# Optimization experiments

Measured on AMD Instinct MI355X. Metric: run time of the kernel, lower is better.

Reference implementation:

```python
import jax, jax.numpy as jnp
import numpy as np

LN_EPS = 1e-5  # torch.nn.LayerNorm default


def setup_inputs() -> dict:
    key = jax.random.key(0)
    ks = jax.random.split(key, 6)
    b, e, c, h, w, m = 4, 16, 256, 32, 64, 1024
    return {
        "x": jax.random.normal(ks[0], (b, e, c, h, w), dtype=jnp.float32),
        "ln_w": jnp.ones((c, h, w), dtype=jnp.float32),
        "ln_b": jnp.zeros((c, h, w), dtype=jnp.float32),
        "w_in": jax.random.normal(ks[1], (c, m), dtype=jnp.float32) * (1.0 / np.sqrt(c)),
        "b_in": jax.random.normal(ks[2], (m,), dtype=jnp.float32) * 0.01,
        "w_out": jax.random.normal(ks[3], (m, c), dtype=jnp.float32) * (1.0 / np.sqrt(m)),
        "b_out": jax.random.normal(ks[4], (c,), dtype=jnp.float32) * 0.01,
        "gamma": jnp.full((c,), 1e-6, dtype=jnp.float32),
    }


def reference(x, ln_w, ln_b, w_in, b_in, w_out, b_out, gamma):
    # LayerNorm over the last 3 dims (c, h, w) with affine params of shape (c, h, w)
    mu = jnp.mean(x, axis=(-3, -2, -1), keepdims=True)
    var = jnp.var(x, axis=(-3, -2, -1), keepdims=True)  # biased, matches torch
    y = (x - mu) * jax.lax.rsqrt(var + LN_EPS)
    y = y * ln_w + ln_b  # broadcast (c,h,w) over (b,e,...)

    # b e c h w -> b e h w c
    y = jnp.moveaxis(y, 2, -1)
    t = jax.nn.gelu(y @ w_in + b_in, approximate=False)  # torch GELU is exact erf
    t = (t @ w_out + b_out) * gamma  # layer scale on channel dim

    # b e h w c -> b e c h w, residual add
    return x + jnp.moveaxis(t, -1, 2)
```

## Files before the change

### kernel.cpp

```cpp
#include <hip/hip_runtime.h>
#include <math.h>

#define NS 64
#define CD 256
#define HW 2048
#define MD 1024
#define SAMPLE (CD * HW)
#define LN_EPS 1e-5f

#define PB 64
#define MC 32
#define NCH (MD / MC)

typedef float f32x4 __attribute__((ext_vector_type(4)));
typedef long i64;
typedef long i64x2 __attribute__((ext_vector_type(2)));

__device__ __forceinline__ int swz(int p) {
  int k = (p ^ (p >> 2)) & 15;
  return ((k & 7) << 4) | (k & 8);
}

__device__ __forceinline__ void gl_lds16(const unsigned char* g, unsigned char* l) {
  __builtin_amdgcn_global_load_lds(
      (const __attribute__((address_space(1))) unsigned char*)g,
      (__attribute__((address_space(3))) unsigned char*)l, 16, 0, 0);
}

__global__ __launch_bounds__(256) void k_prep_stats(
    const float* __restrict__ x, const float* __restrict__ w_in,
    const float* __restrict__ w_out, unsigned char* __restrict__ w_in8p,
    unsigned char* __restrict__ w_out8p, double* __restrict__ partial) {
  if (blockIdx.x < 512) {
    int s = blockIdx.x >> 3, sl = blockIdx.x & 7;
    const float4* p = (const float4*)(x + (size_t)s * SAMPLE + (size_t)sl * 65536);
    double sum = 0.0, ssq = 0.0;
    for (int i = 0; i < 64; ++i) {
      float4 v = p[i * 256 + threadIdx.x];
      sum += (double)v.x + (double)v.y + (double)v.z + (double)v.w;
      ssq += (double)v.x * v.x + (double)v.y * v.y + (double)v.z * v.z + (double)v.w * v.w;
    }
    for (int off = 32; off; off >>= 1) {
      sum += __shfl_down(sum, off);
      ssq += __shfl_down(ssq, off);
    }
    __shared__ double red[4][2];
    int wv = threadIdx.x >> 6, ln = threadIdx.x & 63;
    if (ln == 0) { red[wv][0] = sum; red[wv][1] = ssq; }
    __syncthreads();
    if (threadIdx.x == 0) {
      for (int i = 1; i < 4; ++i) { sum += red[i][0]; ssq += red[i][1]; }
      partial[blockIdx.x * 2] = sum;
      partial[blockIdx.x * 2 + 1] = ssq;
    }
  } else {
    int id = (blockIdx.x - 512) * 256 + threadIdx.x;
    int off = id << 2;
    int ch = off >> 13, r = off & 8191;
    int h = r >> 12; r &= 4095;
    int pr = r >> 10; r &= 1023;
    int lane = r >> 4; r &= 15;
    int lo = r >> 3, j0 = r & 7;
    int kk = pr * 2 + lo;
    if (id < 65536) {
      int m = ch * 32 + h * 16 + (lane & 15);
      int c0 = kk * 32 + (lane >> 4) * 8 + j0;
      float a = w_in[(size_t)(c0 + 0) * MD + m];
      float b = w_in[(size_t)(c0 + 1) * MD + m];
      float c = w_in[(size_t)(c0 + 2) * MD + m];
      float d = w_in[(size_t)(c0 + 3) * MD + m];
      int rr = __builtin_amdgcn_cvt_pk_fp8_f32(a, b, 0, false);
      rr = __builtin_amdgcn_cvt_pk_fp8_f32(c, d, rr, true);
      *(int*)(w_in8p + off) = rr;
    } else {
      off = (id - 65536) << 2;
      ch = off >> 13; r = off & 8191;
      h = r >> 12; r &= 4095;
      pr = r >> 10; r &= 1023;
      lane = r >> 4; r &= 15;
      lo = r >> 3; j0 = r & 7;
      int ct = pr * 2 + lo;
      int c = h * 128 + ct * 16 + (lane & 15);
      int m0 = ch * 32 + (lane >> 4) * 8 + j0;
      float a = w_out[(size_t)(m0 + 0) * CD + c];
      float b = w_out[(size_t)(m0 + 1) * CD + c];
      float cc = w_out[(size_t)(m0 + 2) * CD + c];
      float d = w_out[(size_t)(m0 + 3) * CD + c];
      int rr = __builtin_amdgcn_cvt_pk_fp8_f32(a, b, 0, false);
      rr = __builtin_amdgcn_cvt_pk_fp8_f32(cc, d, rr, true);
      *(int*)(w_out8p + off) = rr;
    }
  }
}

__global__ __launch_bounds__(512, 6) void k_fused(
    const float* __restrict__ x, const float* __restrict__ ln_w, const float* __restrict__ ln_b,
    const float* __restrict__ b_in, const float* __restrict__ b_out, const float* __restrict__ gamma,
    const unsigned char* __restrict__ w_in8p, const unsigned char* __restrict__ w_out8p,
    const double* __restrict__ partial, float* __restrict__ out) {
  __shared__ unsigned char smem[45056];
  unsigned char* Ysh = smem + 8192;

  const int tid = threadIdx.x;
  const int lane = tid & 63, l15 = lane & 15, l4 = lane >> 4;
  const int wv = tid >> 6;
  const int q = wv >> 1, h = wv & 1;
  const int s = blockIdx.x >> 5;
  const int p0 = (blockIdx.x & 31) * PB;
  const size_t xbase = (size_t)s * SAMPLE;

  double sum = 0.0, ssq = 0.0;
  #pragma unroll
  for (int i = 0; i < 8; ++i) {
    sum += partial[s * 16 + i * 2];
    ssq += partial[s * 16 + i * 2 + 1];
  }
  double mean = sum / (double)SAMPLE;
  double var = ssq / (double)SAMPLE - mean * mean;
  const float rstd = (float)(1.0 / sqrt(var + (double)LN_EPS));
  const float a_ln = rstd, c_ln = -(float)mean * rstd;

  gl_lds16(w_in8p + wv * 1024 + lane * 16, smem + 24576 + wv * 1024);
  gl_lds16(w_out8p + wv * 1024 + lane * 16, smem + wv * 1024);

  #pragma unroll
  for (int it = 0; it < 2; ++it) {
    int bid = it * 512 + tid;
    int c0 = (bid >> 4) * 4, pp = (bid & 15) * 4;
    float yv[4][4];
    #pragma unroll
    for (int i = 0; i < 4; ++i) {
      size_t off = (size_t)(c0 + i) * HW + p0 + pp;
      float4 xv = *(const float4*)(x + xbase + off);
      float4 lw = *(const float4*)(ln_w + off);
      float4 lb = *(const float4*)(ln_b + off);
      yv[i][0] = fmaf(fmaf(xv.x, a_ln, c_ln), lw.x, lb.x);
      yv[i][1] = fmaf(fmaf(xv.y, a_ln, c_ln), lw.y, lb.y);
      yv[i][2] = fmaf(fmaf(xv.z, a_ln, c_ln), lw.z, lb.z);
      yv[i][3] = fmaf(fmaf(xv.w, a_ln, c_ln), lw.w, lb.w);
    }
    #pragma unroll
    for (int j = 0; j < 4; ++j) {
      int p = pp + j;
      int r = __builtin_amdgcn_cvt_pk_fp8_f32(yv[0][j], yv[1][j], 0, false);
      r = __builtin_amdgcn_cvt_pk_fp8_f32(yv[2][j], yv[3][j], r, true);
      *(int*)&Ysh[p * 256 + (c0 ^ swz(p))] = r;
    }
  }

  const int strip = q * 16;
  const int pY = strip + l15;
  const int sY = swz(pY);
  f32x4 acc2[8] = {};

  __syncthreads();

  i64 breg[8];
  #pragma unroll
  for (int kk = 0; kk < 8; ++kk)
    breg[kk] = *(const i64*)&Ysh[pY * 256 + ((kk * 32 + l4 * 8) ^ sY)];

  __syncthreads();

  const int exw = ((((h * 16 + l4 * 4) >> 3) ^ (l15 >> 2)) << 3) + ((l4 & 1) * 4);
  const int exw_off = 40960 + q * 512 + l15 * 32 + exw;
  const int exr_off = 40960 + q * 512 + l15 * 32 + ((l4 ^ (l15 >> 2)) << 3);

  for (int ch = 0; ch < NCH; ++ch) {
    if (ch) __syncthreads();

    if (ch + 1 < NCH) {
      const size_t co = (size_t)(ch + 1) * 8192;
      gl_lds16(w_in8p + co + wv * 1024 + lane * 16,
               smem + 24576 + ((ch + 1) & 1) * 8192 + wv * 1024);
      gl_lds16(w_out8p + co + wv * 1024 + lane * 16,
               smem + ((ch + 1) % 3) * 8192 + wv * 1024);
    }

    i64 a2 = 0;
    if (ch) a2 = *(const i64*)(smem + ((ch - 1) & 1) * 2048 + exr_off);

    const unsigned char* W1 = smem + 24576 + (ch & 1) * 8192 + h * 4096;
    f32x4 acc1a = {}, acc1b = {};
    __builtin_amdgcn_s_setprio(1);
    #pragma unroll
    for (int kp = 0; kp < 4; ++kp) {
      i64x2 w = *(const i64x2*)&W1[kp * 1024 + lane * 16];
      acc1a = __builtin_amdgcn_mfma_f32_16x16x32_fp8_fp8(w.x, breg[kp * 2], acc1a, 0, 0, 0);
      acc1b = __builtin_amdgcn_mfma_f32_16x16x32_fp8_fp8(w.y, breg[kp * 2 + 1], acc1b, 0, 0, 0);
    }
    __builtin_amdgcn_s_setprio(0);

    {
      const float4 bi = *(const float4*)&b_in[ch * 32 + h * 16 + l4 * 4];
      float g[4];
      #pragma unroll
      for (int r = 0; r < 4; ++r) {
        float t = acc1a[r] + acc1b[r] + ((const float*)&bi)[r];
        g[r] = t * __builtin_amdgcn_rcpf(1.0f + __expf(-1.702f * t));
      }
      int pk = __builtin_amdgcn_cvt_pk_fp8_f32(g[0], g[1], 0, false);
      pk = __builtin_amdgcn_cvt_pk_fp8_f32(g[2], g[3], pk, true);
      *(int*)(smem + (ch & 1) * 2048 + exw_off) = pk;
    }

    if (ch) {
      const unsigned char* W2 = smem + ((ch - 1) % 3) * 8192 + h * 4096;
      __builtin_amdgcn_s_setprio(1);
      #pragma unroll
      for (int cp = 0; cp < 4; ++cp) {
        i64x2 w = *(const i64x2*)&W2[cp * 1024 + lane * 16];
        acc2[cp * 2] = __builtin_amdgcn_mfma_f32_16x16x32_fp8_fp8(a2, w.x, acc2[cp * 2], 0, 0, 0);
        acc2[cp * 2 + 1] = __builtin_amdgcn_mfma_f32_16x16x32_fp8_fp8(a2, w.y, acc2[cp * 2 + 1], 0, 0, 0);
      }
      __builtin_amdgcn_s_setprio(0);
    }
  }

  __syncthreads();
  {
    const i64 a2 = *(const i64*)(smem + ((NCH - 1) & 1) * 2048 + exr_off);
    const unsigned char* W2 = smem + ((NCH - 1) % 3) * 8192 + h * 4096;
    #pragma unroll
    for (int cp = 0; cp < 4; ++cp) {
      i64x2 w = *(const i64x2*)&W2[cp * 1024 + lane * 16];
      acc2[cp * 2] = __builtin_amdgcn_mfma_f32_16x16x32_fp8_fp8(a2, w.x, acc2[cp * 2], 0, 0, 0);
      acc2[cp * 2 + 1] = __builtin_amdgcn_mfma_f32_16x16x32_fp8_fp8(a2, w.y, acc2[cp * 2 + 1], 0, 0, 0);
    }
  }

  #pragma unroll
  for (int cti = 0; cti < 8; ++cti) {
    int cc = h * 128 + cti * 16 + l15;
    float gm = gamma[cc], bo = b_out[cc];
    int p = p0 + strip + l4 * 4;
    size_t off = xbase + (size_t)cc * HW + p;
    float4 xv = *(const float4*)(x + off);
    float4 o;
    #pragma unroll
    for (int r = 0; r < 4; ++r)
      ((float*)&o)[r] = ((const float*)&xv)[r] + gm * (acc2[cti][r] + bo);
    *(float4*)(out + off) = o;
  }
}

extern "C" void kernel_launch(void* const* d_in, const int* in_sizes, int n_in,
                              void* d_out, int out_size, void* d_ws, size_t ws_size,
                              hipStream_t stream) {
  const float* x = (const float*)d_in[0];
  const float* ln_w = (const float*)d_in[1];
  const float* ln_b = (const float*)d_in[2];
  const float* w_in = (const float*)d_in[3];
  const float* b_in = (const float*)d_in[4];
  const float* w_out = (const float*)d_in[5];
  const float* b_out = (const float*)d_in[6];
  const float* gamma = (const float*)d_in[7];
  float* out = (float*)d_out;

  char* ws = (char*)d_ws;
  unsigned char* w_in8p = (unsigned char*)ws;
  unsigned char* w_out8p = (unsigned char*)(ws + 262144);
  double* partial = (double*)(ws + 524288);

  k_prep_stats<<<1024, 256, 0, stream>>>(x, w_in, w_out, w_in8p, w_out8p, partial);

  k_fused<<<2048, 512, 0, stream>>>(x, ln_w, ln_b, b_in, b_out, gamma,
                                    w_in8p, w_out8p, partial, out);
}
```

Before: 169.8 us.

## Load w_out fragments from global directly and keep Y tile resident in LDS

Stops staging the packed fp8 w_out chunks through a triple-buffered LDS region and has each lane load its w_out fragments straight from global memory (L2-cached) each chunk. Half of the Y operand registers are now re-read from LDS inside the loop instead of being held, so Ysh must stay live and the post-load barrier is dropped. The Y tile moves to offset 0, which shrinks LDS from 45056 to 36864 bytes to raise occupancy and reduce register pressure. In exchange the loop issues global loads with higher latency on the GEMM2 path and adds LDS reads in GEMM1.

```diff
diff --git a/kernel.cpp b/kernel.cpp
--- a/kernel.cpp
+++ b/kernel.cpp
@@ -55,14 +55,14 @@
     }
   } else {
     int id = (blockIdx.x - 512) * 256 + threadIdx.x;
-    int off = id << 2;
-    int ch = off >> 13, r = off & 8191;
-    int h = r >> 12; r &= 4095;
-    int pr = r >> 10; r &= 1023;
-    int lane = r >> 4; r &= 15;
-    int lo = r >> 3, j0 = r & 7;
-    int kk = pr * 2 + lo;
     if (id < 65536) {
+      int off = id << 2;
+      int ch = off >> 13, r = off & 8191;
+      int h = r >> 12; r &= 4095;
+      int pr = r >> 10; r &= 1023;
+      int lane = r >> 4; r &= 15;
+      int lo = r >> 3, j0 = r & 7;
+      int kk = pr * 2 + lo;
       int m = ch * 32 + h * 16 + (lane & 15);
       int c0 = kk * 32 + (lane >> 4) * 8 + j0;
       float a = w_in[(size_t)(c0 + 0) * MD + m];
@@ -73,12 +73,12 @@
       rr = __builtin_amdgcn_cvt_pk_fp8_f32(c, d, rr, true);
       *(int*)(w_in8p + off) = rr;
     } else {
-      off = (id - 65536) << 2;
-      ch = off >> 13; r = off & 8191;
-      h = r >> 12; r &= 4095;
-      pr = r >> 10; r &= 1023;
-      lane = r >> 4; r &= 15;
-      lo = r >> 3; j0 = r & 7;
+      int off = (id - 65536) << 2;
+      int ch = off >> 13, r = off & 8191;
+      int h = r >> 12; r &= 4095;
+      int pr = r >> 10; r &= 1023;
+      int lane = r >> 4; r &= 15;
+      int lo = r >> 3, j0 = r & 7;
       int ct = pr * 2 + lo;
       int c = h * 128 + ct * 16 + (lane & 15);
       int m0 = ch * 32 + (lane >> 4) * 8 + j0;
@@ -98,8 +98,8 @@
     const float* __restrict__ b_in, const float* __restrict__ b_out, const float* __restrict__ gamma,
     const unsigned char* __restrict__ w_in8p, const unsigned char* __restrict__ w_out8p,
     const double* __restrict__ partial, float* __restrict__ out) {
-  __shared__ unsigned char smem[45056];
-  unsigned char* Ysh = smem + 8192;
+  __shared__ unsigned char smem[36864];
+  unsigned char* Ysh = smem;
 
   const int tid = threadIdx.x;
   const int lane = tid & 63, l15 = lane & 15, l4 = lane >> 4;
@@ -120,8 +120,7 @@
   const float rstd = (float)(1.0 / sqrt(var + (double)LN_EPS));
   const float a_ln = rstd, c_ln = -(float)mean * rstd;
 
-  gl_lds16(w_in8p + wv * 1024 + lane * 16, smem + 24576 + wv * 1024);
-  gl_lds16(w_out8p + wv * 1024 + lane * 16, smem + wv * 1024);
+  gl_lds16(w_in8p + wv * 1024 + lane * 16, smem + 16384 + wv * 1024);
 
   #pragma unroll
   for (int it = 0; it < 2; ++it) {
@@ -155,39 +154,50 @@
 
   __syncthreads();
 
-  i64 breg[8];
-  #pragma unroll
-  for (int kk = 0; kk < 8; ++kk)
+  i64 breg[4];
+  #pragma unroll
+  for (int kk = 0; kk < 4; ++kk)
     breg[kk] = *(const i64*)&Ysh[pY * 256 + ((kk * 32 + l4 * 8) ^ sY)];
 
-  __syncthreads();
-
   const int exw = ((((h * 16 + l4 * 4) >> 3) ^ (l15 >> 2)) << 3) + ((l4 & 1) * 4);
-  const int exw_off = 40960 + q * 512 + l15 * 32 + exw;
-  const int exr_off = 40960 + q * 512 + l15 * 32 + ((l4 ^ (l15 >> 2)) << 3);
+  const int exw_off = 32768 + q * 512 + l15 * 32 + exw;
+  const int exr_off = 32768 + q * 512 + l15 * 32 + ((l4 ^ (l15 >> 2)) << 3);
+
+  const unsigned char* W2g = w_out8p + h * 4096 + lane * 16;
 
   for (int ch = 0; ch < NCH; ++ch) {
     if (ch) __syncthreads();
 
     if (ch + 1 < NCH) {
-      const size_t co = (size_t)(ch + 1) * 8192;
-      gl_lds16(w_in8p + co + wv * 1024 + lane * 16,
-               smem + 24576 + ((ch + 1) & 1) * 8192 + wv * 1024);
-      gl_lds16(w_out8p + co + wv * 1024 + lane * 16,
-               smem + ((ch + 1) % 3) * 8192 + wv * 1024);
-    }
-
+      gl_lds16(w_in8p + (size_t)(ch + 1) * 8192 + wv * 1024 + lane * 16,
+               smem + 16384 + ((ch + 1) & 1) * 8192 + wv * 1024);
+    }
+
+    i64x2 w2p[4];
     i64 a2 = 0;
-    if (ch) a2 = *(const i64*)(smem + ((ch - 1) & 1) * 2048 + exr_off);
-
-    const unsigned char* W1 = smem + 24576 + (ch & 1) * 8192 + h * 4096;
+    if (ch) {
+      #pragma unroll
+      for (int cp = 0; cp < 4; ++cp)
+        w2p[cp] = *(const i64x2*)(W2g + (size_t)(ch - 1) * 8192 + cp * 1024);
+      a2 = *(const i64*)(smem + ((ch - 1) & 1) * 2048 + exr_off);
+    }
+
+    const unsigned char* W1 = smem + 16384 + (ch & 1) * 8192 + h * 4096;
     f32x4 acc1a = {}, acc1b = {};
     __builtin_amdgcn_s_setprio(1);
     #pragma unroll
     for (int kp = 0; kp < 4; ++kp) {
       i64x2 w = *(const i64x2*)&W1[kp * 1024 + lane * 16];
-      acc1a = __builtin_amdgcn_mfma_f32_16x16x32_fp8_fp8(w.x, breg[kp * 2], acc1a, 0, 0, 0);
-      acc1b = __builtin_amdgcn_mfma_f32_16x16x32_fp8_fp8(w.y, breg[kp * 2 + 1], acc1b, 0, 0, 0);
+      i64 b0, b1;
+      if (kp < 2) {
+        b0 = breg[kp * 2];
+        b1 = breg[kp * 2 + 1];
+      } else {
+        b0 = *(const i64*)&Ysh[pY * 256 + (((kp * 2) * 32 + l4 * 8) ^ sY)];
+        b1 = *(const i64*)&Ysh[pY * 256 + (((kp * 2 + 1) * 32 + l4 * 8) ^ sY)];
+      }
+      acc1a = __builtin_amdgcn_mfma_f32_16x16x32_fp8_fp8(w.x, b0, acc1a, 0, 0, 0);
+      acc1b = __builtin_amdgcn_mfma_f32_16x16x32_fp8_fp8(w.y, b1, acc1b, 0, 0, 0);
     }
     __builtin_amdgcn_s_setprio(0);
 
@@ -205,13 +215,11 @@
     }
 
     if (ch) {
-      const unsigned char* W2 = smem + ((ch - 1) % 3) * 8192 + h * 4096;
       __builtin_amdgcn_s_setprio(1);
       #pragma unroll
       for (int cp = 0; cp < 4; ++cp) {
-        i64x2 w = *(const i64x2*)&W2[cp * 1024 + lane * 16];
-        acc2[cp * 2] = __builtin_amdgcn_mfma_f32_16x16x32_fp8_fp8(a2, w.x, acc2[cp * 2], 0, 0, 0);
-        acc2[cp * 2 + 1] = __builtin_amdgcn_mfma_f32_16x16x32_fp8_fp8(a2, w.y, acc2[cp * 2 + 1], 0, 0, 0);
+        acc2[cp * 2] = __builtin_amdgcn_mfma_f32_16x16x32_fp8_fp8(a2, w2p[cp].x, acc2[cp * 2], 0, 0, 0);
+        acc2[cp * 2 + 1] = __builtin_amdgcn_mfma_f32_16x16x32_fp8_fp8(a2, w2p[cp].y, acc2[cp * 2 + 1], 0, 0, 0);
       }
       __builtin_amdgcn_s_setprio(0);
     }
@@ -220,10 +228,9 @@
   __syncthreads();
   {
     const i64 a2 = *(const i64*)(smem + ((NCH - 1) & 1) * 2048 + exr_off);
-    const unsigned char* W2 = smem + ((NCH - 1) % 3) * 8192 + h * 4096;
     #pragma unroll
     for (int cp = 0; cp < 4; ++cp) {
-      i64x2 w = *(const i64x2*)&W2[cp * 1024 + lane * 16];
+      i64x2 w = *(const i64x2*)(W2g + (size_t)(NCH - 1) * 8192 + cp * 1024);
       acc2[cp * 2] = __builtin_amdgcn_mfma_f32_16x16x32_fp8_fp8(a2, w.x, acc2[cp * 2], 0, 0, 0);
       acc2[cp * 2 + 1] = __builtin_amdgcn_mfma_f32_16x16x32_fp8_fp8(a2, w.y, acc2[cp * 2 + 1], 0, 0, 0);
     }
```

Measured after the change: 312.5 us. 1.84x slower.
